# Optimization experiments

Hardware: AMD Instinct MI355X
Metric: run time of the kernel (lower is better)

Reference implementation:

```python
import jax, jax.numpy as jnp
import numpy as np

# PyramidAttention (core of UrbanODE): channel=64, reduction=2, ksize=3, level=5,
# stride=1, softmax_scale=10, average=True, res_scale=1, input 32x32.
SCALES = [1.0, 0.9, 0.8, 0.7, 0.6]
SOFTMAX_SCALE = 10.0
ESCAPE_NAN = 1e-4


def _prelu(x, a):
    return jnp.where(x >= 0, x, a * x)


def _conv1x1(x, w, b):
    # x: [B,Cin,H,W], w: [Cout,Cin], b: [Cout]
    return jnp.einsum('oc,bchw->bohw', w, x) + b[None, :, None, None]


def _resize_nearest(x, s):
    # torch F.interpolate(mode='nearest', recompute_scale_factor=True):
    # out = floor(in*s), src_idx = floor(dst*in/out)
    H, W = x.shape[2], x.shape[3]
    oh, ow = int(np.floor(H * s)), int(np.floor(W * s))
    iy = (np.arange(oh) * H) // oh
    ix = (np.arange(ow) * W) // ow
    return x[:, :, iy][:, :, :, ix]


def _patches3(x):
    # 3x3 patches, stride 1, 'same' (pad 1): [B,C,H,W] -> [B,H*W,C,3,3]
    # flatten order matches torch Unfold: (C, kh, kw)
    B, C, H, W = x.shape
    xp = jnp.pad(x, ((0, 0), (0, 0), (1, 1), (1, 1)))
    cols = jnp.stack([xp[:, :, dy:dy + H, dx:dx + W]
                      for dy in range(3) for dx in range(3)], axis=2)  # [B,C,9,H,W]
    return cols.reshape(B, C, 3, 3, H * W).transpose(0, 4, 1, 2, 3)


def _tconv_fold(yi, raw_w):
    # per-sample conv_transpose2d(yi, raw_w, stride=1, padding=1)
    # yi: [N,H,W], raw_w: [N,C,3,3] -> out [C,H,W]
    # transpose-conv (s=1,p=1) == SAME correlation with spatially-flipped kernel
    k = jnp.flip(raw_w, (-2, -1)).transpose(1, 0, 2, 3)  # [C,N,3,3]
    return jax.lax.conv_general_dilated(
        yi[None], k, (1, 1), ((1, 1), (1, 1)),
        dimension_numbers=('NCHW', 'OIHW', 'NCHW'))[0]


def setup_inputs() -> dict:
    key = jax.random.key(0)
    ks = jax.random.split(key, 8)
    B, C, H, W = 32, 64, 32, 32
    C2 = C // 2
    return {
        'x': jax.random.normal(ks[0], (B, C, H, W), jnp.float32),
        'w_base': 0.05 * jax.random.normal(ks[1], (C2, C), jnp.float32),
        'b_base': jnp.zeros((C2,), jnp.float32),
        'a_base': jnp.full((1,), 0.25, jnp.float32),
        'w_match': 0.05 * jax.random.normal(ks[2], (C2, C), jnp.float32),
        'b_match': jnp.zeros((C2,), jnp.float32),
        'a_match': jnp.full((1,), 0.25, jnp.float32),
        'w_asm': 0.05 * jax.random.normal(ks[3], (C, C), jnp.float32),
        'b_asm': jnp.zeros((C,), jnp.float32),
        'a_asm': jnp.full((1,), 0.25, jnp.float32),
    }


def reference(x, w_base, b_base, a_base, w_match, b_match, a_match,
              w_asm, b_asm, a_asm):
    B, C, H, W = x.shape
    match_base = _prelu(_conv1x1(x, w_base, b_base), a_base)  # [B,C/2,H,W]

    wi_list, raw_list = [], []
    for s in SCALES:
        ref = x if s == 1.0 else _resize_nearest(x, s)
        base = _prelu(_conv1x1(ref, w_asm, b_asm), a_asm)      # [B,C,h,w]
        raw_list.append(_patches3(base))                        # [B,hw,C,3,3]
        refm = _prelu(_conv1x1(ref, w_match, b_match), a_match)  # [B,C/2,h,w]
        wi_list.append(_patches3(refm))                         # [B,hw,C/2,3,3]
    wi = jnp.concatenate(wi_list, axis=1)        # [B,N,C/2,3,3], N=3278
    raw_w = jnp.concatenate(raw_list, axis=1)    # [B,N,C,3,3]

    # per-filter L2 normalization (escape_NaN)
    norm = jnp.sqrt(jnp.sum(wi * wi, axis=(2, 3, 4), keepdims=True))
    wi_n = wi / jnp.maximum(norm, ESCAPE_NAN)

    # correlation of query patches with dynamic filters: batched GEMM
    N = wi.shape[1]
    xp = _patches3(match_base).reshape(B, H * W, -1)   # [B,HW,C/2*9]
    yi = jnp.einsum('bnk,bpk->bnp', wi_n.reshape(B, N, -1), xp)  # [B,N,HW]
    yi = jax.nn.softmax(yi * SOFTMAX_SCALE, axis=1)
    yi = yi.reshape(B, N, H, W)

    out = jax.vmap(_tconv_fold)(yi, raw_w) / 4.0       # [B,C,H,W]
    return out + x  # res_scale = 1
```

## Files before the change

kernel.cpp:

```cpp
#include <hip/hip_runtime.h>
#include <hip/hip_bf16.h>
#include <math.h>

#define BB 32
#define CC 64
#define C2 32
#define HH 32
#define WW 32
#define HW 1024
#define NTOT 3278
#define NPAD2 3328
#define NT26 26
#define NT64 52

typedef __bf16   bf16x8 __attribute__((ext_vector_type(8)));
typedef _Float16 half8  __attribute__((ext_vector_type(8)));
typedef float    f32x4  __attribute__((ext_vector_type(4)));

__device__ __constant__ int SC_SIZE[5] = {32, 28, 25, 22, 19};
__device__ __constant__ int SC_OFF[6]  = {0, 1024, 1808, 2433, 2917, 3278};

#define XS_STR 65
#define WS_STR 132
__global__ void __launch_bounds__(256, 1) k_feats(
        const float* __restrict__ x,
        const float* __restrict__ wb, const float* __restrict__ bb, const float* __restrict__ ab,
        const float* __restrict__ wm, const float* __restrict__ bm, const float* __restrict__ am,
        const float* __restrict__ wa, const float* __restrict__ ba, const float* __restrict__ aa,
        _Float16* __restrict__ mft, _Float16* __restrict__ rft,
        __bf16* __restrict__ basef,
        float* __restrict__ mbss, float* __restrict__ rmss) {
    __shared__ float Xs[64 * XS_STR];
    __shared__ float Wls[64 * WS_STR];
    __shared__ float bsh[128];
    __shared__ float ash3[3];
    int tid = threadIdx.x;
    int g0 = blockIdx.x * 64;
    int b = g0 >> 10, p0 = g0 & 1023;

    const float* xb = x + (size_t)b * CC * HW + p0;
    for (int i = tid; i < 64 * 64; i += 256) {
        int c = i >> 6, p = i & 63;
        Xs[c * XS_STR + p] = xb[(size_t)c * HW + p];
    }
    for (int i = tid; i < 128 * 64; i += 256) {
        int o = i >> 6, c = i & 63;
        float w = (o < 32) ? wb[o * CC + c] : (o < 64) ? wm[(o - 32) * CC + c] : wa[(o - 64) * CC + c];
        Wls[c * WS_STR + o] = w;
    }
    if (tid < 128) bsh[tid] = (tid < 32) ? bb[tid] : (tid < 64) ? bm[tid - 32] : ba[tid - 64];
    if (tid == 128) ash3[0] = ab[0];
    if (tid == 129) ash3[1] = am[0];
    if (tid == 130) ash3[2] = aa[0];
    __syncthreads();

    int p = tid & 63, og = tid >> 6;
    int o0 = og * 32;
    float acc[32];
#pragma unroll
    for (int oi = 0; oi < 32; ++oi) acc[oi] = bsh[o0 + oi];
    for (int c = 0; c < 64; ++c) {
        float xv = Xs[c * XS_STR + p];
        const float* wr = &Wls[c * WS_STR + o0];
#pragma unroll
        for (int oi = 0; oi < 32; ++oi) acc[oi] += wr[oi] * xv;
    }
    int pp = p0 + p;
    if (og < 2) {
        float alpha = ash3[og], ss = 0.f;
        half8 hv[4];
#pragma unroll
        for (int oi = 0; oi < 32; ++oi) {
            float v = acc[oi] >= 0.f ? acc[oi] : alpha * acc[oi];
            ss += v * v;
            hv[oi >> 3][oi & 7] = (_Float16)v;
        }
        _Float16* d = (og == 0 ? mft : rft) + ((size_t)b * HW + pp) * 32;
#pragma unroll
        for (int q = 0; q < 4; ++q) *(half8*)&d[q * 8] = hv[q];
        if (og == 0) mbss[(size_t)b * HW + pp] = ss;
        else         rmss[(size_t)b * HW + pp] = ss;
    } else {
        float alpha = ash3[2];
        int ob = o0 - 64;
#pragma unroll
        for (int oi = 0; oi < 32; ++oi) {
            float v = acc[oi] >= 0.f ? acc[oi] : alpha * acc[oi];
            basef[((size_t)b * CC + ob + oi) * HW + pp] = (__bf16)v;
        }
    }
}

__global__ void k_nbr(int* __restrict__ nbr_pos) {
    int n = blockIdx.x * blockDim.x + threadIdx.x;
    if (n >= NTOT) return;
    int s = 0;
    while (s < 4 && n >= SC_OFF[s + 1]) ++s;
    int q = n - SC_OFF[s];
    int hs = SC_SIZE[s];
    int ny = q / hs, nx = q % hs;
    for (int dy = 0; dy < 3; ++dy)
        for (int dx = 0; dx < 3; ++dx) {
            int yy = ny + dy - 1, xx = nx + dx - 1;
            int pos = -1;
            if (yy >= 0 && yy < hs && xx >= 0 && xx < hs)
                pos = ((yy * HH) / hs) * WW + (xx * WW) / hs;
            nbr_pos[(dy * 3 + dx) * NTOT + n] = pos;
        }
}

__global__ void k_qnorm(const float* __restrict__ mbss, float* __restrict__ qub) {
    int t = blockIdx.x * blockDim.x + threadIdx.x;
    int b = t >> 10, p = t & 1023;
    int y = p >> 5, x = p & 31;
    float s = 0.f;
#pragma unroll
    for (int dy = 0; dy < 3; ++dy)
#pragma unroll
        for (int dx = 0; dx < 3; ++dx) {
            int yy = y + dy - 1, xx = x + dx - 1;
            if (yy >= 0 && yy < HH && xx >= 0 && xx < WW)
                s += mbss[(size_t)b * HW + yy * WW + xx];
        }
    qub[t] = 10.0f * sqrtf(s);
}

__global__ void k_norms(const float* __restrict__ rmss, const int* __restrict__ nbr_pos,
                        float* __restrict__ sinv) {
    int t = blockIdx.x * blockDim.x + threadIdx.x;
    if (t >= BB * NTOT) return;
    int b = t / NTOT, n = t % NTOT;
    float sum = 0.f;
#pragma unroll
    for (int kk = 0; kk < 9; ++kk) {
        int pos = nbr_pos[kk * NTOT + n];
        if (pos >= 0) sum += rmss[(size_t)b * HW + pos];
    }
    sinv[t] = 10.0f / fmaxf(sqrtf(sum), 1e-4f);
}

__global__ void k_vgather(const __bf16* __restrict__ basef, const int* __restrict__ nbr_pos,
                          __bf16* __restrict__ Vb, int b0) {
    int c = blockIdx.x, cb = blockIdx.y;
    int tid = threadIdx.x;
    __shared__ __bf16 row[HW];
    const __bf16* src = basef + ((size_t)(b0 + cb) * CC + c) * HW;
    for (int i = tid; i < HW / 8; i += 256)
        *(bf16x8*)&row[i * 8] = *(const bf16x8*)&src[i * 8];
    __syncthreads();
    for (int t = tid; t < 9 * (NPAD2 / 8); t += 256) {
        int kk = t / (NPAD2 / 8), nq = t - kk * (NPAD2 / 8);
        int n0 = nq * 8;
        const int* nb = &nbr_pos[kk * NTOT];
        bf16x8 v8;
#pragma unroll
        for (int u = 0; u < 8; ++u) {
            int n = n0 + u;
            __bf16 v = (__bf16)0.f;
            if (n < NTOT) {
                int pos = nb[n];
                if (pos >= 0) v = row[pos];
            }
            v8[u] = v;
        }
        int m = c * 9 + kk;
        int nt = n0 >> 6;
        int j0s = (((n0 & 63) >> 3) ^ (m & 7)) << 3;
        *(bf16x8*)&Vb[(((size_t)cb * NT64 + nt) * 576 + m) * 64 + j0s] = v8;
    }
}

__global__ void k_corr_mfma(const _Float16* __restrict__ mft, const _Float16* __restrict__ rft,
                            const int* __restrict__ nbr_pos,
                            const float* __restrict__ sinv, const float* __restrict__ qub,
                            __bf16* __restrict__ tbuf, float* __restrict__ partS, int b0) {
    int ptile = blockIdx.x;
    int ntile = blockIdx.y;
    int cb    = blockIdx.z;
    int tid  = threadIdx.x;
    int lane = tid & 63, wave = tid >> 6;
    int row16 = lane & 15, quad = lane >> 4;
    int p0 = ptile * 64, n0 = ntile * 128;

    __shared__ _Float16 Ah[64 * 40];
    __shared__ _Float16 Bh[128 * 40];
    __shared__ int   nbrs[9][128];
    __shared__ float sMub[64];
    __shared__ float redS[4][64];
    __shared__ __bf16 Tls[4][16 * 40];

    if (tid < 64) sMub[tid] = qub[(size_t)(b0 + cb) * HW + p0 + tid];
    for (int i = tid; i < 9 * 128; i += 256) {
        int kk = i >> 7, j = i & 127;
        int n = n0 + j;
        nbrs[kk][j] = (n < NTOT) ? nbr_pos[kk * NTOT + n] : -1;
    }

    const _Float16* mh = mft + (size_t)(b0 + cb) * HW * 32;
    const _Float16* rh = rft + (size_t)(b0 + cb) * HW * 32;

    f32x4 acc[4][2];
#pragma unroll
    for (int i = 0; i < 4; ++i)
#pragma unroll
        for (int j = 0; j < 2; ++j) acc[i][j] = (f32x4){0.f, 0.f, 0.f, 0.f};

    half8 zero8;
#pragma unroll
    for (int u = 0; u < 8; ++u) zero8[u] = (_Float16)0.f;

    __syncthreads();

    half8 pA, pB[2];
    int ap = tid >> 2, ac = (tid & 3) * 8;
    int pg = p0 + ap, ay = pg >> 5, ax = pg & 31;
    auto gatherA = [&](int kk, half8* dst) {
        int py = ay + kk / 3 - 1, px = ax + (kk % 3) - 1;
        bool ok = (py >= 0 && py < HH && px >= 0 && px < WW);
        *dst = ok ? *(const half8*)(mh + (size_t)(py * WW + px) * 32 + ac) : zero8;
    };
    auto gatherB = [&](int kk, half8* dst) {
#pragma unroll
        for (int it = 0; it < 2; ++it) {
            int tt = tid + it * 256;
            int bn = tt >> 2, bc = (tt & 3) * 8;
            int pos = nbrs[kk][bn];
            dst[it] = (pos >= 0) ? *(const half8*)(rh + (size_t)pos * 32 + bc) : zero8;
        }
    };

    gatherA(0, &pA);
    gatherB(0, pB);

    for (int kk = 0; kk < 9; ++kk) {
        __syncthreads();
        *(half8*)&Ah[ap * 40 + ac] = pA;
#pragma unroll
        for (int it = 0; it < 2; ++it) {
            int tt = tid + it * 256;
            int rrow = tt >> 2, rc = (tt & 3) * 8;
            *(half8*)&Bh[rrow * 40 + rc] = pB[it];
        }
        if (kk < 8) {
            gatherA(kk + 1, &pA);
            gatherB(kk + 1, pB);
        }
        __syncthreads();
        half8 af[4], bf[2];
#pragma unroll
        for (int m = 0; m < 4; ++m)
            af[m] = *(const half8*)&Ah[(m * 16 + row16) * 40 + quad * 8];
#pragma unroll
        for (int nb = 0; nb < 2; ++nb)
            bf[nb] = *(const half8*)&Bh[(wave * 32 + nb * 16 + row16) * 40 + quad * 8];
#pragma unroll
        for (int m = 0; m < 4; ++m)
#pragma unroll
            for (int nb = 0; nb < 2; ++nb)
                acc[m][nb] = __builtin_amdgcn_mfma_f32_16x16x32_f16(af[m], bf[nb], acc[m][nb], 0, 0, 0);
    }

    int nn[2];
    float sv[2];
    bool valid[2];
#pragma unroll
    for (int nb = 0; nb < 2; ++nb) {
        nn[nb] = n0 + wave * 32 + nb * 16 + row16;
        valid[nb] = nn[nb] < NTOT;
        sv[nb] = valid[nb] ? sinv[(size_t)(b0 + cb) * NTOT + nn[nb]] : 0.f;
    }
    float sm[4][4];
#pragma unroll
    for (int m = 0; m < 4; ++m)
#pragma unroll
        for (int r = 0; r < 4; ++r) sm[m][r] = 0.f;

    int tr = lane >> 2, tc = (lane & 3) * 8;
#pragma unroll
    for (int m = 0; m < 4; ++m) {
#pragma unroll
        for (int nb = 0; nb < 2; ++nb) {
#pragma unroll
            for (int r = 0; r < 4; ++r) {
                float mub = sMub[m * 16 + quad * 4 + r];
                float e = valid[nb] ? __expf(acc[m][nb][r] * sv[nb] - mub) : 0.f;
                Tls[wave][(quad * 4 + r) * 40 + nb * 16 + row16] = (__bf16)e;
                sm[m][r] += e;
            }
        }
        bf16x8 v = *(const bf16x8*)&Tls[wave][tr * 40 + tc];
        int nc = wave * 32 + tc;
        int nglob = n0 + nc;
        int nt = nglob >> 6, j0 = nglob & 63;
        int j0s = ((j0 >> 3) ^ (tr & 7)) << 3;
        int p = p0 + m * 16 + tr;
        *(bf16x8*)&tbuf[(((size_t)cb * NT64 + nt) * HW + p) * 64 + j0s] = v;
    }

#pragma unroll
    for (int msk = 1; msk < 16; msk <<= 1)
#pragma unroll
        for (int m = 0; m < 4; ++m)
#pragma unroll
            for (int r = 0; r < 4; ++r) sm[m][r] += __shfl_xor(sm[m][r], msk, 64);
    if (row16 == 0)
#pragma unroll
        for (int m = 0; m < 4; ++m)
#pragma unroll
            for (int r = 0; r < 4; ++r) redS[wave][m * 16 + quad * 4 + r] = sm[m][r];
    __syncthreads();
    if (wave == 0 && row16 == 0) {
#pragma unroll
        for (int m = 0; m < 4; ++m)
#pragma unroll
            for (int r = 0; r < 4; ++r) {
                int p = m * 16 + quad * 4 + r;
                float S = redS[0][p] + redS[1][p] + redS[2][p] + redS[3][p];
                partS[((size_t)cb * HW + p0 + p) * NT26 + ntile] = S;
            }
    }
}

__global__ void k_rowsum(const float* __restrict__ partS, float* __restrict__ fin) {
    int row = blockIdx.x * 256 + threadIdx.x;
    float s = 0.f;
#pragma unroll
    for (int nt = 0; nt < NT26; ++nt) s += partS[(size_t)row * NT26 + nt];
    fin[row] = 1.0f / fmaxf(s, 1e-38f);
}

__device__ __forceinline__ void gload16(const void* g, void* l) {
    __builtin_amdgcn_global_load_lds(
        (const __attribute__((address_space(1))) void*)g,
        (__attribute__((address_space(3))) void*)l, 16, 0, 0);
}

#define A_KSTRIDE (576 * 64 * 2)
#define B_KSTRIDE (1024 * 64 * 2)
#define FM 192
#define FP 128

__global__ void __launch_bounds__(512, 4) k_fold_mfma(
        const __bf16* __restrict__ Vb, const __bf16* __restrict__ tbuf,
        const float* __restrict__ fin, __bf16* __restrict__ outacc) {
    int ptile = blockIdx.x;
    int mtile = blockIdx.y;
    int cb    = blockIdx.z;
    int tid  = threadIdx.x;
    int lane = tid & 63, wave = tid >> 6;
    int row16 = lane & 15, quad = lane >> 4;
    int wrM = wave >> 2, wrN = wave & 3;

    __shared__ __bf16 Als[2][FM * 64];
    __shared__ __bf16 Bls[2][FP * 64];

    const char* Ag = (const char*)(Vb   + (((size_t)cb * NT64) * 576  + (size_t)mtile * FM) * 64);
    const char* Bg = (const char*)(tbuf + (((size_t)cb * NT64) * 1024 + (size_t)ptile * FP) * 64);

    f32x4 acc[6][2];
#pragma unroll
    for (int i = 0; i < 6; ++i)
#pragma unroll
        for (int j = 0; j < 2; ++j) acc[i][j] = (f32x4){0.f, 0.f, 0.f, 0.f};

    int lo16 = lane * 16;
    auto stage = [&](int sb, int kt) {
#pragma unroll
        for (int i = 0; i < 5; ++i) {
            int q = wave * 5 + i;
            if (q < 24) {
                gload16(Ag + (size_t)kt * A_KSTRIDE + q * 1024 + lo16,
                        (char*)&Als[sb][0] + q * 1024);
            } else {
                gload16(Bg + (size_t)kt * B_KSTRIDE + (q - 24) * 1024 + lo16,
                        (char*)&Bls[sb][0] + (q - 24) * 1024);
            }
        }
    };

    int sg = row16 & 7;
    auto compute = [&](int sb) {
#pragma unroll
        for (int kh = 0; kh < 2; ++kh) {
            int ko = ((kh * 4 + quad) ^ sg) << 3;
            bf16x8 af[6], bf[2];
#pragma unroll
            for (int mb = 0; mb < 6; ++mb)
                af[mb] = *(const bf16x8*)&Als[sb][(wrM * 96 + mb * 16 + row16) * 64 + ko];
#pragma unroll
            for (int pbi = 0; pbi < 2; ++pbi)
                bf[pbi] = *(const bf16x8*)&Bls[sb][(wrN * 32 + pbi * 16 + row16) * 64 + ko];
#pragma unroll
            for (int mb = 0; mb < 6; ++mb)
#pragma unroll
                for (int pbi = 0; pbi < 2; ++pbi)
                    acc[mb][pbi] = __builtin_amdgcn_mfma_f32_16x16x32_bf16(af[mb], bf[pbi], acc[mb][pbi], 0, 0, 0);
        }
    };

    stage(0, 0);
    __syncthreads();
    int cur = 0;
    for (int kt = 0; kt < NT64; ++kt) {
        if (kt + 1 < NT64) stage(cur ^ 1, kt + 1);
        compute(cur);
        __syncthreads();
        cur ^= 1;
    }

    float fsc[2];
#pragma unroll
    for (int pbi = 0; pbi < 2; ++pbi)
        fsc[pbi] = fin[(size_t)cb * HW + ptile * FP + wrN * 32 + pbi * 16 + row16];
#pragma unroll
    for (int mb = 0; mb < 6; ++mb)
#pragma unroll
        for (int pbi = 0; pbi < 2; ++pbi) {
#pragma unroll
            for (int r = 0; r < 4; ++r) {
                int mg = mtile * FM + wrM * 96 + mb * 16 + quad * 4 + r;
                int pg = ptile * FP + wrN * 32 + pbi * 16 + row16;
                outacc[((size_t)cb * 576 + mg) * HW + pg] = (__bf16)(acc[mb][pbi][r] * fsc[pbi]);
            }
        }
}

__global__ void k_epilogue(const float* __restrict__ x, const __bf16* __restrict__ outacc,
                           float* __restrict__ out, int b0) {
    int t = blockIdx.x * blockDim.x + threadIdx.x;
    int cb = t >> 16;
    int c = (t >> 10) & 63;
    int p = t & 1023;
    int b = b0 + cb;
    int y = p >> 5, xx = p & 31;
    float acc = 0.f;
#pragma unroll
    for (int ky = 0; ky < 3; ++ky)
#pragma unroll
        for (int kx = 0; kx < 3; ++kx) {
            int py = y + 1 - ky, px = xx + 1 - kx;
            if (py >= 0 && py < HH && px >= 0 && px < WW)
                acc += (float)outacc[((size_t)cb * 576 + c * 9 + ky * 3 + kx) * HW + py * WW + px];
        }
    size_t o = ((size_t)b * CC + c) * HW + p;
    out[o] = x[o] + 0.25f * acc;
}

extern "C" void kernel_launch(void* const* d_in, const int* in_sizes, int n_in,
                              void* d_out, int out_size, void* d_ws, size_t ws_size,
                              hipStream_t stream) {
    const float* x       = (const float*)d_in[0];
    const float* w_base  = (const float*)d_in[1];
    const float* b_base  = (const float*)d_in[2];
    const float* a_base  = (const float*)d_in[3];
    const float* w_match = (const float*)d_in[4];
    const float* b_match = (const float*)d_in[5];
    const float* a_match = (const float*)d_in[6];
    const float* w_asm   = (const float*)d_in[7];
    const float* b_asm   = (const float*)d_in[8];
    const float* a_asm   = (const float*)d_in[9];
    float* out = (float*)d_out;

    const size_t fixed = ((size_t)BB * HW * 32 * 2) * 2 + ((size_t)BB * CC * HW * 2) +
                         ((size_t)BB * HW * 4) * 3 + ((size_t)BB * NTOT * 4) +
                         ((size_t)9 * NTOT * 4) + 65536;
    const size_t perCB = ((size_t)HW * NPAD2 * 2) + ((size_t)HW * NT26 * 4) +
                         ((size_t)HW * 4) + ((size_t)576 * NPAD2 * 2) +
                         ((size_t)576 * HW * 2) + 65536;
    int CB = 32;
    while (CB > 1 && fixed + perCB * CB > ws_size) CB >>= 1;

    char* ws = (char*)d_ws;
    size_t off = 0;
    auto alloc_b = [&](size_t bytes) {
        void* p = (void*)(ws + off);
        off += bytes;
        off = (off + 255) & ~(size_t)255;
        return p;
    };
    _Float16* mft   = (_Float16*)alloc_b((size_t)BB * HW * 32 * 2);
    _Float16* rft   = (_Float16*)alloc_b((size_t)BB * HW * 32 * 2);
    __bf16* base_f  = (__bf16*)alloc_b((size_t)BB * CC * HW * 2);
    float*  mbss    = (float*)alloc_b((size_t)BB * HW * 4);
    float*  rmss    = (float*)alloc_b((size_t)BB * HW * 4);
    float*  qub     = (float*)alloc_b((size_t)BB * HW * 4);
    float*  sinv    = (float*)alloc_b((size_t)BB * NTOT * 4);
    int*    nbr_pos = (int*)alloc_b((size_t)9 * NTOT * 4);
    __bf16* tbuf    = (__bf16*)alloc_b((size_t)CB * HW * NPAD2 * 2);
    float*  partS   = (float*)alloc_b((size_t)CB * HW * NT26 * 4);
    float*  fin     = (float*)alloc_b((size_t)CB * HW * 4);
    __bf16* Vb      = (__bf16*)alloc_b((size_t)CB * 576 * NPAD2 * 2);
    __bf16* outacc  = (__bf16*)alloc_b((size_t)CB * 576 * HW * 2);
    if (off > ws_size) return;

    k_feats<<<BB * HW / 64, 256, 0, stream>>>(
        x, w_base, b_base, a_base, w_match, b_match, a_match, w_asm, b_asm, a_asm,
        mft, rft, base_f, mbss, rmss);
    k_nbr<<<(NTOT + 255) / 256, 256, 0, stream>>>(nbr_pos);
    k_qnorm<<<BB * HW / 256, 256, 0, stream>>>(mbss, qub);
    k_norms<<<(BB * NTOT + 255) / 256, 256, 0, stream>>>(rmss, nbr_pos, sinv);

    for (int b0 = 0; b0 < BB; b0 += CB) {
        k_corr_mfma<<<dim3(16, NT26, CB), 256, 0, stream>>>(
            mft, rft, nbr_pos, sinv, qub, tbuf, partS, b0);
        k_rowsum<<<CB * HW / 256, 256, 0, stream>>>(partS, fin);
        k_vgather<<<dim3(CC, CB), 256, 0, stream>>>(base_f, nbr_pos, Vb, b0);
        k_fold_mfma<<<dim3(8, 3, CB), 512, 0, stream>>>(Vb, tbuf, fin, outacc);
        k_epilogue<<<CB * CC * HW / 256, 256, 0, stream>>>(x, outacc, out, b0);
    }
}
```

Before: 579.0 us.

## Enlarge correlation tile to 128x128 with 512-thread blocks and precomputed A positions

The correlation GEMM kernel now covers 128 query positions per block instead of 64 and uses eight waves arranged 2x4, so each gathered B tile (128 filters) is reused by twice as many rows. This halves the redundant gathers of the filter patches. Query neighbor offsets are precomputed into shared memory, replacing per-iteration bounds arithmetic. The costs are more shared memory per block, fewer blocks in the grid, and 512-thread blocks that may lower occupancy.

```diff
diff --git a/kernel.cpp b/kernel.cpp
--- a/kernel.cpp
+++ b/kernel.cpp
@@ -170,30 +170,36 @@
     }
 }
 
-__global__ void k_corr_mfma(const _Float16* __restrict__ mft, const _Float16* __restrict__ rft,
-                            const int* __restrict__ nbr_pos,
-                            const float* __restrict__ sinv, const float* __restrict__ qub,
-                            __bf16* __restrict__ tbuf, float* __restrict__ partS, int b0) {
+__global__ void __launch_bounds__(512) k_corr_mfma(
+        const _Float16* __restrict__ mft, const _Float16* __restrict__ rft,
+        const int* __restrict__ nbr_pos,
+        const float* __restrict__ sinv, const float* __restrict__ qub,
+        __bf16* __restrict__ tbuf, float* __restrict__ partS, int b0) {
     int ptile = blockIdx.x;
     int ntile = blockIdx.y;
     int cb    = blockIdx.z;
     int tid  = threadIdx.x;
     int lane = tid & 63, wave = tid >> 6;
     int row16 = lane & 15, quad = lane >> 4;
-    int p0 = ptile * 64, n0 = ntile * 128;
-
-    __shared__ _Float16 Ah[64 * 40];
+    int wrP = wave >> 2, wrN = wave & 3;
+    int p0 = ptile * 128, n0 = ntile * 128;
+
+    __shared__ _Float16 Ah[128 * 40];
     __shared__ _Float16 Bh[128 * 40];
     __shared__ int   nbrs[9][128];
-    __shared__ float sMub[64];
-    __shared__ float redS[4][64];
-    __shared__ __bf16 Tls[4][16 * 40];
-
-    if (tid < 64) sMub[tid] = qub[(size_t)(b0 + cb) * HW + p0 + tid];
-    for (int i = tid; i < 9 * 128; i += 256) {
+    __shared__ int   posA[9][128];
+    __shared__ float sMub[128];
+    __shared__ float redS[8][64];
+    __shared__ __bf16 Tls[8][16 * 40];
+
+    if (tid < 128) sMub[tid] = qub[(size_t)(b0 + cb) * HW + p0 + tid];
+    for (int i = tid; i < 9 * 128; i += 512) {
         int kk = i >> 7, j = i & 127;
         int n = n0 + j;
         nbrs[kk][j] = (n < NTOT) ? nbr_pos[kk * NTOT + n] : -1;
+        int pg = p0 + j;
+        int py = (pg >> 5) + kk / 3 - 1, px = (pg & 31) + kk % 3 - 1;
+        posA[kk][j] = (py >= 0 && py < HH && px >= 0 && px < WW) ? (py * WW + px) : -1;
     }
 
     const _Float16* mh = mft + (size_t)(b0 + cb) * HW * 32;
@@ -211,48 +217,36 @@
 
     __syncthreads();
 
-    half8 pA, pB[2];
-    int ap = tid >> 2, ac = (tid & 3) * 8;
-    int pg = p0 + ap, ay = pg >> 5, ax = pg & 31;
+    half8 pA, pB;
+    int ar = tid >> 2, ac = (tid & 3) * 8;
     auto gatherA = [&](int kk, half8* dst) {
-        int py = ay + kk / 3 - 1, px = ax + (kk % 3) - 1;
-        bool ok = (py >= 0 && py < HH && px >= 0 && px < WW);
-        *dst = ok ? *(const half8*)(mh + (size_t)(py * WW + px) * 32 + ac) : zero8;
+        int pa = posA[kk][ar];
+        *dst = (pa >= 0) ? *(const half8*)(mh + (size_t)pa * 32 + ac) : zero8;
     };
     auto gatherB = [&](int kk, half8* dst) {
-#pragma unroll
-        for (int it = 0; it < 2; ++it) {
-            int tt = tid + it * 256;
-            int bn = tt >> 2, bc = (tt & 3) * 8;
-            int pos = nbrs[kk][bn];
-            dst[it] = (pos >= 0) ? *(const half8*)(rh + (size_t)pos * 32 + bc) : zero8;
-        }
+        int pos = nbrs[kk][ar];
+        *dst = (pos >= 0) ? *(const half8*)(rh + (size_t)pos * 32 + ac) : zero8;
     };
 
     gatherA(0, &pA);
-    gatherB(0, pB);
+    gatherB(0, &pB);
 
     for (int kk = 0; kk < 9; ++kk) {
         __syncthreads();
-        *(half8*)&Ah[ap * 40 + ac] = pA;
-#pragma unroll
-        for (int it = 0; it < 2; ++it) {
-            int tt = tid + it * 256;
-            int rrow = tt >> 2, rc = (tt & 3) * 8;
-            *(half8*)&Bh[rrow * 40 + rc] = pB[it];
-        }
+        *(half8*)&Ah[ar * 40 + ac] = pA;
+        *(half8*)&Bh[ar * 40 + ac] = pB;
         if (kk < 8) {
             gatherA(kk + 1, &pA);
-            gatherB(kk + 1, pB);
+            gatherB(kk + 1, &pB);
         }
         __syncthreads();
         half8 af[4], bf[2];
 #pragma unroll
         for (int m = 0; m < 4; ++m)
-            af[m] = *(const half8*)&Ah[(m * 16 + row16) * 40 + quad * 8];
+            af[m] = *(const half8*)&Ah[(wrP * 64 + m * 16 + row16) * 40 + quad * 8];
 #pragma unroll
         for (int nb = 0; nb < 2; ++nb)
-            bf[nb] = *(const half8*)&Bh[(wave * 32 + nb * 16 + row16) * 40 + quad * 8];
+            bf[nb] = *(const half8*)&Bh[(wrN * 32 + nb * 16 + row16) * 40 + quad * 8];
 #pragma unroll
         for (int m = 0; m < 4; ++m)
 #pragma unroll
@@ -265,7 +259,7 @@
     bool valid[2];
 #pragma unroll
     for (int nb = 0; nb < 2; ++nb) {
-        nn[nb] = n0 + wave * 32 + nb * 16 + row16;
+        nn[nb] = n0 + wrN * 32 + nb * 16 + row16;
         valid[nb] = nn[nb] < NTOT;
         sv[nb] = valid[nb] ? sinv[(size_t)(b0 + cb) * NTOT + nn[nb]] : 0.f;
     }
@@ -282,18 +276,17 @@
         for (int nb = 0; nb < 2; ++nb) {
 #pragma unroll
             for (int r = 0; r < 4; ++r) {
-                float mub = sMub[m * 16 + quad * 4 + r];
+                float mub = sMub[wrP * 64 + m * 16 + quad * 4 + r];
                 float e = valid[nb] ? __expf(acc[m][nb][r] * sv[nb] - mub) : 0.f;
                 Tls[wave][(quad * 4 + r) * 40 + nb * 16 + row16] = (__bf16)e;
                 sm[m][r] += e;
             }
         }
         bf16x8 v = *(const bf16x8*)&Tls[wave][tr * 40 + tc];
-        int nc = wave * 32 + tc;
-        int nglob = n0 + nc;
+        int nglob = n0 + wrN * 32 + tc;
         int nt = nglob >> 6, j0 = nglob & 63;
         int j0s = ((j0 >> 3) ^ (tr & 7)) << 3;
-        int p = p0 + m * 16 + tr;
+        int p = p0 + wrP * 64 + m * 16 + tr;
         *(bf16x8*)&tbuf[(((size_t)cb * NT64 + nt) * HW + p) * 64 + j0s] = v;
     }
 
@@ -309,14 +302,15 @@
 #pragma unroll
             for (int r = 0; r < 4; ++r) redS[wave][m * 16 + quad * 4 + r] = sm[m][r];
     __syncthreads();
-    if (wave == 0 && row16 == 0) {
+    if ((wave == 0 || wave == 4) && row16 == 0) {
 #pragma unroll
         for (int m = 0; m < 4; ++m)
 #pragma unroll
             for (int r = 0; r < 4; ++r) {
                 int p = m * 16 + quad * 4 + r;
-                float S = redS[0][p] + redS[1][p] + redS[2][p] + redS[3][p];
-                partS[((size_t)cb * HW + p0 + p) * NT26 + ntile] = S;
+                float S = redS[wrP * 4 + 0][p] + redS[wrP * 4 + 1][p] +
+                          redS[wrP * 4 + 2][p] + redS[wrP * 4 + 3][p];
+                partS[((size_t)cb * HW + p0 + wrP * 64 + p) * NT26 + ntile] = S;
             }
     }
 }
@@ -501,7 +495,7 @@
     k_norms<<<(BB * NTOT + 255) / 256, 256, 0, stream>>>(rmss, nbr_pos, sinv);
 
     for (int b0 = 0; b0 < BB; b0 += CB) {
-        k_corr_mfma<<<dim3(16, NT26, CB), 256, 0, stream>>>(
+        k_corr_mfma<<<dim3(8, NT26, CB), 512, 0, stream>>>(
             mft, rft, nbr_pos, sinv, qub, tbuf, partS, b0);
         k_rowsum<<<CB * HW / 256, 256, 0, stream>>>(partS, fin);
         k_vgather<<<dim3(CC, CB), 256, 0, stream>>>(base_f, nbr_pos, Vb, b0);
```

After: 573.9 us. No clear change (-0.9%).
